# Optimization experiments

Measured on AMD Instinct MI355X. Metric: run time of the kernel, lower is better.

The kernel has to match this reference:

```python
import jax, jax.numpy as jnp
import numpy as np

N = 50000
E = 800000
F_IN = 128
HID = 64
HEADS = 4
NUM_TYPES = 1
NEG_SLOPE = 0.2


def setup_inputs() -> dict:
    key = jax.random.key(0)
    ks = jax.random.split(key, 20)
    s = 0.05
    inp = {
        "node_features": jax.random.normal(ks[0], (N, F_IN), jnp.float32),
        "node_types": jax.random.randint(ks[1], (N,), 0, NUM_TYPES, jnp.int32),
        "edge_index": jax.random.randint(ks[2], (2, E), 0, N, jnp.int32),
        # params
        "type_emb": jax.random.normal(ks[3], (NUM_TYPES, HID), jnp.float32) * s,
        "proj_w": jax.random.normal(ks[4], (F_IN, HID), jnp.float32) * s,
        "proj_b": jnp.zeros((HID,), jnp.float32),
        # GAT layer 0: in=64 -> heads*64, concat=True
        "lin_w0": jax.random.normal(ks[5], (HID, HEADS * HID), jnp.float32) * s,
        "att_src0": jax.random.normal(ks[6], (HEADS, HID), jnp.float32) * s,
        "att_dst0": jax.random.normal(ks[7], (HEADS, HID), jnp.float32) * s,
        "bias0": jnp.zeros((HEADS * HID,), jnp.float32),
        "ln_g0": jnp.ones((HEADS * HID,), jnp.float32),
        "ln_b0": jnp.zeros((HEADS * HID,), jnp.float32),
        # GAT layer 1: in=256 -> heads*64, concat=False (mean over heads)
        "lin_w1": jax.random.normal(ks[8], (HEADS * HID, HEADS * HID), jnp.float32) * s,
        "att_src1": jax.random.normal(ks[9], (HEADS, HID), jnp.float32) * s,
        "att_dst1": jax.random.normal(ks[10], (HEADS, HID), jnp.float32) * s,
        "bias1": jnp.zeros((HID,), jnp.float32),
        "ln_g1": jnp.ones((HID,), jnp.float32),
        "ln_b1": jnp.zeros((HID,), jnp.float32),
    }
    return inp


def _layer_norm(x, g, b, eps=1e-5):
    mu = jnp.mean(x, axis=-1, keepdims=True)
    var = jnp.mean(jnp.square(x - mu), axis=-1, keepdims=True)
    return (x - mu) * jax.lax.rsqrt(var + eps) * g + b


def _gat_conv(x, src, dst, lin_w, att_src, att_dst, bias, concat):
    # PyG GATConv: linear -> per-edge additive attention -> segment softmax over
    # incoming edges -> weighted scatter-sum. Self-loops already in src/dst.
    n = x.shape[0]
    H, C = att_src.shape
    h = (x @ lin_w).reshape(n, H, C)            # [N,H,C]
    a_s = jnp.sum(h * att_src[None], axis=-1)   # [N,H]
    a_d = jnp.sum(h * att_dst[None], axis=-1)   # [N,H]
    a = jax.nn.leaky_relu(a_s[src] + a_d[dst], NEG_SLOPE)  # [E,H]
    m = jax.ops.segment_max(a, dst, num_segments=n)
    e = jnp.exp(a - m[dst])
    z = jax.ops.segment_sum(e, dst, num_segments=n)
    alpha = e / z[dst]                           # [E,H]
    msg = h[src] * alpha[..., None]              # [E,H,C]
    out = jax.ops.segment_sum(msg, dst, num_segments=n)  # [N,H,C]
    if concat:
        out = out.reshape(n, H * C)
    else:
        out = out.mean(axis=1)
    return out + bias


def reference(node_features, node_types, edge_index,
              type_emb, proj_w, proj_b,
              lin_w0, att_src0, att_dst0, bias0, ln_g0, ln_b0,
              lin_w1, att_src1, att_dst1, bias1, ln_g1, ln_b1):
    n = node_features.shape[0]
    # add self loops (PyG GATConv default add_self_loops=True)
    loop = jnp.arange(n, dtype=edge_index.dtype)
    src = jnp.concatenate([edge_index[0], loop])
    dst = jnp.concatenate([edge_index[1], loop])

    x = node_features @ proj_w + proj_b + type_emb[node_types]  # [N,64]

    # layer 0: no residual (i == 0)
    x = _gat_conv(x, src, dst, lin_w0, att_src0, att_dst0, bias0, concat=True)
    x = jax.nn.relu(_layer_norm(x, ln_g0, ln_b0))  # [N,256]; dropout = identity (eval)

    # layer 1: residual shape [N,256] != output [N,64] -> residual skipped
    x = _gat_conv(x, src, dst, lin_w1, att_src1, att_dst1, bias1, concat=False)
    x = jax.nn.relu(_layer_norm(x, ln_g1, ln_b1))  # [N,64]
    return x
```

## Files before the change

kernel.cpp:

```cpp
#include <hip/hip_runtime.h>


#define BLK 256
#define FB  2048

typedef __bf16 bf16x8 __attribute__((ext_vector_type(8)));
typedef __bf16 bf16x4 __attribute__((ext_vector_type(4)));
typedef float  f32x4  __attribute__((ext_vector_type(4)));


__device__ __forceinline__ void pack_body(const float* __restrict__ w,
                                          __bf16* __restrict__ wp,
                                          int K, int NC, int idx) {
  const int tot = (K >> 3) * NC;
  if (idx >= tot) return;
  int g = idx / NC, c = idx - g * NC;
#pragma unroll
  for (int j = 0; j < 8; ++j)
    wp[(size_t)idx * 8 + j] = (__bf16)w[(g * 8 + j) * NC + c];
}

__device__ __forceinline__ void proj_body(
    int bid, const float* __restrict__ nf, const int* __restrict__ types,
    const __bf16* __restrict__ pwp, const float* __restrict__ pb,
    const float* __restrict__ emb, __bf16* __restrict__ x0, int n) {
  const int t = threadIdx.x, w = t >> 6, l = t & 63;
  const int l15 = l & 15, lg = l >> 4;
  const int mbase = bid * 64 + w * 16;
  f32x4 acc[4] = {};
  const int ar = mbase + l15;
  const bool av = ar < n;
#pragma unroll
  for (int ks = 0; ks < 4; ++ks) {
    bf16x8 a = {};
    if (av) {
      const float* ap = nf + (size_t)ar * 128 + ks * 32 + lg * 8;
      float4 f0 = *(const float4*)(ap);
      float4 f1 = *(const float4*)(ap + 4);
      a[0] = (__bf16)f0.x; a[1] = (__bf16)f0.y; a[2] = (__bf16)f0.z; a[3] = (__bf16)f0.w;
      a[4] = (__bf16)f1.x; a[5] = (__bf16)f1.y; a[6] = (__bf16)f1.z; a[7] = (__bf16)f1.w;
    }
#pragma unroll
    for (int nt = 0; nt < 4; ++nt) {
      int c = nt * 16 + l15;
      int g = ks * 4 + lg;
      bf16x8 b = *(const bf16x8*)(pwp + ((size_t)g * 64 + c) * 8);
      acc[nt] = __builtin_amdgcn_mfma_f32_16x16x32_bf16(a, b, acc[nt], 0, 0, 0);
    }
  }
#pragma unroll
  for (int reg = 0; reg < 4; ++reg) {
    int row = mbase + lg * 4 + reg;
    if (row < n) {
      int ty = types[row];
#pragma unroll
      for (int nt = 0; nt < 4; ++nt) {
        int c = nt * 16 + l15;
        x0[(size_t)row * 64 + c] = (__bf16)(acc[nt][reg] + pb[c] + emb[ty * 64 + c]);
      }
    }
  }
}

template <int K>
__device__ __forceinline__ void lin_body(
    int bid, const __bf16* __restrict__ X, const __bf16* __restrict__ Wp,
    const float* __restrict__ att_s, const float* __restrict__ att_d,
    __bf16* __restrict__ H, float* __restrict__ as_, float* __restrict__ ad_, int n) {
  const int t = threadIdx.x, w = t >> 6, l = t & 63;
  const int l15 = l & 15, lg = l >> 4;
  const int m0 = bid * 64;

  float asv[4], adv[4];
#pragma unroll
  for (int nt = 0; nt < 4; ++nt) {
    int c = w * 64 + nt * 16 + l15;
    asv[nt] = att_s[c];
    adv[nt] = att_d[c];
  }

  f32x4 acc[4][4] = {};
  int rr[4];
  bool vv[4];
#pragma unroll
  for (int mt = 0; mt < 4; ++mt) { rr[mt] = m0 + mt * 16 + l15; vv[mt] = rr[mt] < n; }
  const bf16x8 zf = {};

  for (int ks = 0; ks < K / 32; ++ks) {
    bf16x8 a[4];
#pragma unroll
    for (int mt = 0; mt < 4; ++mt)
      a[mt] = vv[mt] ? *(const bf16x8*)(X + (size_t)rr[mt] * K + ks * 32 + lg * 8) : zf;
    bf16x8 b[4];
#pragma unroll
    for (int nt = 0; nt < 4; ++nt) {
      int c = w * 64 + nt * 16 + l15;
      int g = ks * 4 + lg;
      b[nt] = *(const bf16x8*)(Wp + ((size_t)g * 256 + c) * 8);
    }
#pragma unroll
    for (int nt = 0; nt < 4; ++nt)
#pragma unroll
      for (int mt = 0; mt < 4; ++mt)
        acc[mt][nt] = __builtin_amdgcn_mfma_f32_16x16x32_bf16(a[mt], b[nt], acc[mt][nt], 0, 0, 0);
  }

#pragma unroll
  for (int mt = 0; mt < 4; ++mt) {
#pragma unroll
    for (int reg = 0; reg < 4; ++reg) {
      int row = m0 + mt * 16 + lg * 4 + reg;
      bool vr = row < n;
      float s = 0.f, d = 0.f;
      if (vr) {
#pragma unroll
        for (int nt = 0; nt < 4; ++nt) {
          float cv = acc[mt][nt][reg];
          H[(size_t)row * 256 + w * 64 + nt * 16 + l15] = (__bf16)cv;
          s = fmaf(cv, asv[nt], s);
          d = fmaf(cv, adv[nt], d);
        }
      }
#pragma unroll
      for (int o = 8; o; o >>= 1) { s += __shfl_xor(s, o); d += __shfl_xor(d, o); }
      if (l15 == 0 && vr) { as_[row * 4 + w] = s; ad_[row * 4 + w] = d; }
    }
  }
}


__global__ __launch_bounds__(BLK) void k_prep(
    const float* __restrict__ pw, const float* __restrict__ w0,
    const float* __restrict__ w1, __bf16* __restrict__ pwp,
    __bf16* __restrict__ w0p, __bf16* __restrict__ w1p,
    int* __restrict__ cnt, int* __restrict__ sidx, int n, int nchunks) {
  int b = blockIdx.x;
  const int t = threadIdx.x;
  if (b < nchunks) {
    int i = b * BLK + t;
    if (i < n) { cnt[i] = 1; sidx[(size_t)i << 6] = i; }
    return;
  }
  b -= nchunks;
  if (b < 4)  { pack_body(pw, pwp, 128, 64,  b * BLK + t); return; }
  b -= 4;
  if (b < 8)  { pack_body(w0, w0p, 64, 256,  b * BLK + t); return; }
  b -= 8;
  pack_body(w1, w1p, 256, 256, b * BLK + t);
}

__global__ __launch_bounds__(BLK) void k_fill_proj(
    const int* __restrict__ src, const int* __restrict__ dst,
    int* __restrict__ cnt, int* __restrict__ sidx, int E,
    const float* __restrict__ nf, const int* __restrict__ types,
    const __bf16* __restrict__ pwp, const float* __restrict__ pb,
    const float* __restrict__ emb, __bf16* __restrict__ x0, int n) {
  if (blockIdx.x < FB) {
    for (int e = blockIdx.x * BLK + threadIdx.x; e < E; e += FB * BLK) {
      int s = src[e], d = dst[e];
      int slot = atomicAdd(&cnt[d], 1);
      if (slot < 64) sidx[((size_t)d << 6) + slot] = s;
    }
    return;
  }
  proj_body(blockIdx.x - FB, nf, types, pwp, pb, emb, x0, n);
}

__global__ __launch_bounds__(BLK) void k_lin64(
    const __bf16* __restrict__ X, const __bf16* __restrict__ Wp,
    const float* __restrict__ att_s, const float* __restrict__ att_d,
    __bf16* __restrict__ H, float* __restrict__ as_, float* __restrict__ ad_, int n) {
  lin_body<64>(blockIdx.x, X, Wp, att_s, att_d, H, as_, ad_, n);
}

__global__ __launch_bounds__(BLK) void k_lin256(
    const __bf16* __restrict__ X, const __bf16* __restrict__ Wp,
    const float* __restrict__ att_s, const float* __restrict__ att_d,
    __bf16* __restrict__ H, float* __restrict__ as_, float* __restrict__ ad_, int n) {
  lin_body<256>(blockIdx.x, X, Wp, att_s, att_d, H, as_, ad_, n);
}


__global__ __launch_bounds__(BLK) void k_agg0(
    const int* __restrict__ cntA, const int* __restrict__ sidx,
    const float* __restrict__ as_, const float* __restrict__ ad_,
    const __bf16* __restrict__ h0,
    const float* __restrict__ bias, const float* __restrict__ g,
    const float* __restrict__ b, __bf16* __restrict__ x1, int n) {
  const int lane = threadIdx.x & 63;
  const int wid = (blockIdx.x * BLK + threadIdx.x) >> 6;
  const int nw = (gridDim.x * BLK) >> 6;
  const int hsel = lane >> 4;
  const float4 bias4 = ((const float4*)bias)[lane];
  const float4 g4 = ((const float4*)g)[lane];
  const float4 b4 = ((const float4*)b)[lane];
  for (int d = wid; d < n; d += nw) {
    int cnt = cntA[d]; if (cnt > 64) cnt = 64;
    const int* sp = sidx + ((size_t)d << 6);
    const float adv = ad_[d * 4 + hsel];
    float ax = 0.f, ay = 0.f, az = 0.f, aw = 0.f, z = 0.f;
    int j = 0;
    for (; j + 4 <= cnt; j += 4) {
      int4 s4 = *(const int4*)(sp + j);
      int s0 = __builtin_amdgcn_readfirstlane(s4.x);
      int s1 = __builtin_amdgcn_readfirstlane(s4.y);
      int s2 = __builtin_amdgcn_readfirstlane(s4.z);
      int s3 = __builtin_amdgcn_readfirstlane(s4.w);
      float q0 = as_[s0 * 4 + hsel], q1 = as_[s1 * 4 + hsel];
      float q2 = as_[s2 * 4 + hsel], q3 = as_[s3 * 4 + hsel];
      bf16x4 v0 = *(const bf16x4*)(h0 + (size_t)s0 * 256 + lane * 4);
      bf16x4 v1 = *(const bf16x4*)(h0 + (size_t)s1 * 256 + lane * 4);
      bf16x4 v2 = *(const bf16x4*)(h0 + (size_t)s2 * 256 + lane * 4);
      bf16x4 v3 = *(const bf16x4*)(h0 + (size_t)s3 * 256 + lane * 4);
      float a;
      a = q0 + adv; a = fmaxf(a, 0.2f * a); float e0 = __expf(a);
      a = q1 + adv; a = fmaxf(a, 0.2f * a); float e1 = __expf(a);
      a = q2 + adv; a = fmaxf(a, 0.2f * a); float e2 = __expf(a);
      a = q3 + adv; a = fmaxf(a, 0.2f * a); float e3 = __expf(a);
      z += (e0 + e1) + (e2 + e3);
      ax = fmaf(e0, (float)v0[0], ax); ay = fmaf(e0, (float)v0[1], ay);
      az = fmaf(e0, (float)v0[2], az); aw = fmaf(e0, (float)v0[3], aw);
      ax = fmaf(e1, (float)v1[0], ax); ay = fmaf(e1, (float)v1[1], ay);
      az = fmaf(e1, (float)v1[2], az); aw = fmaf(e1, (float)v1[3], aw);
      ax = fmaf(e2, (float)v2[0], ax); ay = fmaf(e2, (float)v2[1], ay);
      az = fmaf(e2, (float)v2[2], az); aw = fmaf(e2, (float)v2[3], aw);
      ax = fmaf(e3, (float)v3[0], ax); ay = fmaf(e3, (float)v3[1], ay);
      az = fmaf(e3, (float)v3[2], az); aw = fmaf(e3, (float)v3[3], aw);
    }
    for (; j < cnt; ++j) {
      int s = __builtin_amdgcn_readfirstlane(sp[j]);
      float a = as_[s * 4 + hsel] + adv; a = fmaxf(a, 0.2f * a);
      float e = __expf(a);
      z += e;
      bf16x4 hv = *(const bf16x4*)(h0 + (size_t)s * 256 + lane * 4);
      ax = fmaf(e, (float)hv[0], ax); ay = fmaf(e, (float)hv[1], ay);
      az = fmaf(e, (float)hv[2], az); aw = fmaf(e, (float)hv[3], aw);
    }
    float rz = 1.f / z;
    float vx = ax * rz + bias4.x, vy = ay * rz + bias4.y;
    float vz = az * rz + bias4.z, vw = aw * rz + bias4.w;
    float s1 = vx + vy + vz + vw;
#pragma unroll
    for (int o = 32; o; o >>= 1) s1 += __shfl_xor(s1, o);
    float mu = s1 * (1.f / 256.f);
    float dx = vx - mu, dy = vy - mu, dz = vz - mu, dw = vw - mu;
    float q = dx * dx + dy * dy + dz * dz + dw * dw;
#pragma unroll
    for (int o = 32; o; o >>= 1) q += __shfl_xor(q, o);
    float is = rsqrtf(q * (1.f / 256.f) + 1e-5f);
    bf16x4 o4;
    o4[0] = (__bf16)fmaxf(dx * is * g4.x + b4.x, 0.f);
    o4[1] = (__bf16)fmaxf(dy * is * g4.y + b4.y, 0.f);
    o4[2] = (__bf16)fmaxf(dz * is * g4.z + b4.z, 0.f);
    o4[3] = (__bf16)fmaxf(dw * is * g4.w + b4.w, 0.f);
    *(bf16x4*)(x1 + (size_t)d * 256 + lane * 4) = o4;
  }
}

__global__ __launch_bounds__(BLK) void k_agg1(
    const int* __restrict__ cntA, const int* __restrict__ sidx,
    const float* __restrict__ as_, const float* __restrict__ ad_,
    const __bf16* __restrict__ h1,
    const float* __restrict__ bias, const float* __restrict__ g,
    const float* __restrict__ b, float* __restrict__ out, int n) {
  const int lane = threadIdx.x & 63;
  const int wid = (blockIdx.x * BLK + threadIdx.x) >> 6;
  const int nw = (gridDim.x * BLK) >> 6;
  const int hsel = lane >> 4;
  const int p = lane & 15;
  const float4 bias4 = ((const float4*)bias)[p];
  const float4 g4 = ((const float4*)g)[p];
  const float4 b4 = ((const float4*)b)[p];
  for (int d = wid; d < n; d += nw) {
    int cnt = cntA[d]; if (cnt > 64) cnt = 64;
    const int* sp = sidx + ((size_t)d << 6);
    const float adv = ad_[d * 4 + hsel];
    float ax = 0.f, ay = 0.f, az = 0.f, aw = 0.f, z = 0.f;
    int j = 0;
    for (; j + 4 <= cnt; j += 4) {
      int4 s4 = *(const int4*)(sp + j);
      int s0 = __builtin_amdgcn_readfirstlane(s4.x);
      int s1 = __builtin_amdgcn_readfirstlane(s4.y);
      int s2 = __builtin_amdgcn_readfirstlane(s4.z);
      int s3 = __builtin_amdgcn_readfirstlane(s4.w);
      float q0 = as_[s0 * 4 + hsel], q1 = as_[s1 * 4 + hsel];
      float q2 = as_[s2 * 4 + hsel], q3 = as_[s3 * 4 + hsel];
      bf16x4 v0 = *(const bf16x4*)(h1 + (size_t)s0 * 256 + lane * 4);
      bf16x4 v1 = *(const bf16x4*)(h1 + (size_t)s1 * 256 + lane * 4);
      bf16x4 v2 = *(const bf16x4*)(h1 + (size_t)s2 * 256 + lane * 4);
      bf16x4 v3 = *(const bf16x4*)(h1 + (size_t)s3 * 256 + lane * 4);
      float a;
      a = q0 + adv; a = fmaxf(a, 0.2f * a); float e0 = __expf(a);
      a = q1 + adv; a = fmaxf(a, 0.2f * a); float e1 = __expf(a);
      a = q2 + adv; a = fmaxf(a, 0.2f * a); float e2 = __expf(a);
      a = q3 + adv; a = fmaxf(a, 0.2f * a); float e3 = __expf(a);
      z += (e0 + e1) + (e2 + e3);
      ax = fmaf(e0, (float)v0[0], ax); ay = fmaf(e0, (float)v0[1], ay);
      az = fmaf(e0, (float)v0[2], az); aw = fmaf(e0, (float)v0[3], aw);
      ax = fmaf(e1, (float)v1[0], ax); ay = fmaf(e1, (float)v1[1], ay);
      az = fmaf(e1, (float)v1[2], az); aw = fmaf(e1, (float)v1[3], aw);
      ax = fmaf(e2, (float)v2[0], ax); ay = fmaf(e2, (float)v2[1], ay);
      az = fmaf(e2, (float)v2[2], az); aw = fmaf(e2, (float)v2[3], aw);
      ax = fmaf(e3, (float)v3[0], ax); ay = fmaf(e3, (float)v3[1], ay);
      az = fmaf(e3, (float)v3[2], az); aw = fmaf(e3, (float)v3[3], aw);
    }
    for (; j < cnt; ++j) {
      int s = __builtin_amdgcn_readfirstlane(sp[j]);
      float a = as_[s * 4 + hsel] + adv; a = fmaxf(a, 0.2f * a);
      float e = __expf(a);
      z += e;
      bf16x4 hv = *(const bf16x4*)(h1 + (size_t)s * 256 + lane * 4);
      ax = fmaf(e, (float)hv[0], ax); ay = fmaf(e, (float)hv[1], ay);
      az = fmaf(e, (float)hv[2], az); aw = fmaf(e, (float)hv[3], aw);
    }
    float rz = 1.f / z;
    ax *= rz; ay *= rz; az *= rz; aw *= rz;
#pragma unroll
    for (int o = 16; o <= 32; o <<= 1) {
      ax += __shfl_xor(ax, o); ay += __shfl_xor(ay, o);
      az += __shfl_xor(az, o); aw += __shfl_xor(aw, o);
    }
    float vx = 0.25f * ax + bias4.x, vy = 0.25f * ay + bias4.y;
    float vz = 0.25f * az + bias4.z, vw = 0.25f * aw + bias4.w;
    float s1 = vx + vy + vz + vw;
#pragma unroll
    for (int o = 8; o; o >>= 1) s1 += __shfl_xor(s1, o);
    float mu = s1 * (1.f / 64.f);
    float dx = vx - mu, dy = vy - mu, dz = vz - mu, dw = vw - mu;
    float q = dx * dx + dy * dy + dz * dz + dw * dw;
#pragma unroll
    for (int o = 8; o; o >>= 1) q += __shfl_xor(q, o);
    float is = rsqrtf(q * (1.f / 64.f) + 1e-5f);
    if (lane < 16) {
      float4 o4;
      o4.x = fmaxf(dx * is * g4.x + b4.x, 0.f);
      o4.y = fmaxf(dy * is * g4.y + b4.y, 0.f);
      o4.z = fmaxf(dz * is * g4.z + b4.z, 0.f);
      o4.w = fmaxf(dw * is * g4.w + b4.w, 0.f);
      ((float4*)(out + (size_t)d * 64))[p] = o4;
    }
  }
}

extern "C" void kernel_launch(void* const* d_in, const int* in_sizes, int n_in,
                              void* d_out, int out_size, void* d_ws, size_t ws_size,
                              hipStream_t stream) {
  const float* nf    = (const float*)d_in[0];
  const int*   types = (const int*)d_in[1];
  const int*   ei    = (const int*)d_in[2];
  const float* emb   = (const float*)d_in[3];
  const float* pw    = (const float*)d_in[4];
  const float* pb    = (const float*)d_in[5];
  const float* w0    = (const float*)d_in[6];
  const float* asrc0 = (const float*)d_in[7];
  const float* adst0 = (const float*)d_in[8];
  const float* b0    = (const float*)d_in[9];
  const float* g0    = (const float*)d_in[10];
  const float* be0   = (const float*)d_in[11];
  const float* w1    = (const float*)d_in[12];
  const float* asrc1 = (const float*)d_in[13];
  const float* adst1 = (const float*)d_in[14];
  const float* b1    = (const float*)d_in[15];
  const float* g1    = (const float*)d_in[16];
  const float* be1   = (const float*)d_in[17];

  const int n = in_sizes[0] / 128;
  const int E = in_sizes[2] / 2;
  const int* srcI = ei;
  const int* dstI = ei + E;

  float* W = (float*)d_ws;
  size_t o = 0;
  __bf16* x0  = (__bf16*)(W + o); o += (size_t)n * 32;
  __bf16* h   = (__bf16*)(W + o); o += (size_t)n * 128;
  __bf16* x1  = (__bf16*)(W + o); o += (size_t)n * 128;
  float* as_ = W + o;             o += (size_t)n * 4;
  float* ad_ = W + o;             o += (size_t)n * 4;
  __bf16* w0p = (__bf16*)(W + o); o += 64 * 256 / 2;
  __bf16* w1p = (__bf16*)(W + o); o += 256 * 256 / 2;
  __bf16* pwp = (__bf16*)(W + o); o += 128 * 64 / 2;
  int* I = (int*)(W + o);
  size_t io = 0;
  int* cnt  = I + io; io += n;
  int* sidx = I + io; io += (size_t)n * 64;

  const int nchunks = (n + BLK - 1) / BLK;
  const int mgrid = (n + 63) / 64;
  const int agrid = (n * 64 + BLK - 1) / BLK;

  k_prep<<<nchunks + 44, BLK, 0, stream>>>(pw, w0, w1, pwp, w0p, w1p, cnt, sidx, n, nchunks);
  k_fill_proj<<<FB + mgrid, BLK, 0, stream>>>(srcI, dstI, cnt, sidx, E,
                                              nf, types, pwp, pb, emb, x0, n);
  k_lin64<<<mgrid, BLK, 0, stream>>>(x0, w0p, asrc0, adst0, h, as_, ad_, n);
  k_agg0<<<agrid, BLK, 0, stream>>>(cnt, sidx, as_, ad_, h, b0, g0, be0, x1, n);
  k_lin256<<<mgrid, BLK, 0, stream>>>(x1, w1p, asrc1, adst1, h, as_, ad_, n);
  k_agg1<<<agrid, BLK, 0, stream>>>(cnt, sidx, as_, ad_, h, b1, g1, be1,
                                    (float*)d_out, n);
}
```

Before: 258.1 us.

## Fuse input projection with layer-0 linear via LDS and batch edge-fill atomics

Merges the input projection and the layer-0 GAT linear into one kernel. The projected 64-wide tile is staged in shared memory instead of being written to and reread from global memory, which removes one launch and the x0 round trip. The edge-fill part now uses fewer blocks and issues four independent edge loads and atomics per thread iteration to raise memory-level parallelism. The trade-off is extra LDS use and possibly lower occupancy for the projection blocks, and fewer fill blocks may reduce overlap with the MFMA work.

```diff
diff --git a/kernel.cpp b/kernel.cpp
--- a/kernel.cpp
+++ b/kernel.cpp
@@ -2,7 +2,7 @@
 
 
 #define BLK 256
-#define FB  2048
+#define FB  768
 
 typedef __bf16 bf16x8 __attribute__((ext_vector_type(8)));
 typedef __bf16 bf16x4 __attribute__((ext_vector_type(4)));
@@ -18,114 +18,6 @@
 #pragma unroll
   for (int j = 0; j < 8; ++j)
     wp[(size_t)idx * 8 + j] = (__bf16)w[(g * 8 + j) * NC + c];
-}
-
-__device__ __forceinline__ void proj_body(
-    int bid, const float* __restrict__ nf, const int* __restrict__ types,
-    const __bf16* __restrict__ pwp, const float* __restrict__ pb,
-    const float* __restrict__ emb, __bf16* __restrict__ x0, int n) {
-  const int t = threadIdx.x, w = t >> 6, l = t & 63;
-  const int l15 = l & 15, lg = l >> 4;
-  const int mbase = bid * 64 + w * 16;
-  f32x4 acc[4] = {};
-  const int ar = mbase + l15;
-  const bool av = ar < n;
-#pragma unroll
-  for (int ks = 0; ks < 4; ++ks) {
-    bf16x8 a = {};
-    if (av) {
-      const float* ap = nf + (size_t)ar * 128 + ks * 32 + lg * 8;
-      float4 f0 = *(const float4*)(ap);
-      float4 f1 = *(const float4*)(ap + 4);
-      a[0] = (__bf16)f0.x; a[1] = (__bf16)f0.y; a[2] = (__bf16)f0.z; a[3] = (__bf16)f0.w;
-      a[4] = (__bf16)f1.x; a[5] = (__bf16)f1.y; a[6] = (__bf16)f1.z; a[7] = (__bf16)f1.w;
-    }
-#pragma unroll
-    for (int nt = 0; nt < 4; ++nt) {
-      int c = nt * 16 + l15;
-      int g = ks * 4 + lg;
-      bf16x8 b = *(const bf16x8*)(pwp + ((size_t)g * 64 + c) * 8);
-      acc[nt] = __builtin_amdgcn_mfma_f32_16x16x32_bf16(a, b, acc[nt], 0, 0, 0);
-    }
-  }
-#pragma unroll
-  for (int reg = 0; reg < 4; ++reg) {
-    int row = mbase + lg * 4 + reg;
-    if (row < n) {
-      int ty = types[row];
-#pragma unroll
-      for (int nt = 0; nt < 4; ++nt) {
-        int c = nt * 16 + l15;
-        x0[(size_t)row * 64 + c] = (__bf16)(acc[nt][reg] + pb[c] + emb[ty * 64 + c]);
-      }
-    }
-  }
-}
-
-template <int K>
-__device__ __forceinline__ void lin_body(
-    int bid, const __bf16* __restrict__ X, const __bf16* __restrict__ Wp,
-    const float* __restrict__ att_s, const float* __restrict__ att_d,
-    __bf16* __restrict__ H, float* __restrict__ as_, float* __restrict__ ad_, int n) {
-  const int t = threadIdx.x, w = t >> 6, l = t & 63;
-  const int l15 = l & 15, lg = l >> 4;
-  const int m0 = bid * 64;
-
-  float asv[4], adv[4];
-#pragma unroll
-  for (int nt = 0; nt < 4; ++nt) {
-    int c = w * 64 + nt * 16 + l15;
-    asv[nt] = att_s[c];
-    adv[nt] = att_d[c];
-  }
-
-  f32x4 acc[4][4] = {};
-  int rr[4];
-  bool vv[4];
-#pragma unroll
-  for (int mt = 0; mt < 4; ++mt) { rr[mt] = m0 + mt * 16 + l15; vv[mt] = rr[mt] < n; }
-  const bf16x8 zf = {};
-
-  for (int ks = 0; ks < K / 32; ++ks) {
-    bf16x8 a[4];
-#pragma unroll
-    for (int mt = 0; mt < 4; ++mt)
-      a[mt] = vv[mt] ? *(const bf16x8*)(X + (size_t)rr[mt] * K + ks * 32 + lg * 8) : zf;
-    bf16x8 b[4];
-#pragma unroll
-    for (int nt = 0; nt < 4; ++nt) {
-      int c = w * 64 + nt * 16 + l15;
-      int g = ks * 4 + lg;
-      b[nt] = *(const bf16x8*)(Wp + ((size_t)g * 256 + c) * 8);
-    }
-#pragma unroll
-    for (int nt = 0; nt < 4; ++nt)
-#pragma unroll
-      for (int mt = 0; mt < 4; ++mt)
-        acc[mt][nt] = __builtin_amdgcn_mfma_f32_16x16x32_bf16(a[mt], b[nt], acc[mt][nt], 0, 0, 0);
-  }
-
-#pragma unroll
-  for (int mt = 0; mt < 4; ++mt) {
-#pragma unroll
-    for (int reg = 0; reg < 4; ++reg) {
-      int row = m0 + mt * 16 + lg * 4 + reg;
-      bool vr = row < n;
-      float s = 0.f, d = 0.f;
-      if (vr) {
-#pragma unroll
-        for (int nt = 0; nt < 4; ++nt) {
-          float cv = acc[mt][nt][reg];
-          H[(size_t)row * 256 + w * 64 + nt * 16 + l15] = (__bf16)cv;
-          s = fmaf(cv, asv[nt], s);
-          d = fmaf(cv, adv[nt], d);
-        }
-      }
-#pragma unroll
-      for (int o = 8; o; o >>= 1) { s += __shfl_xor(s, o); d += __shfl_xor(d, o); }
-      if (l15 == 0 && vr) { as_[row * 4 + w] = s; ad_[row * 4 + w] = d; }
-    }
-  }
 }
 
 
@@ -149,35 +41,197 @@
   pack_body(w1, w1p, 256, 256, b * BLK + t);
 }
 
-__global__ __launch_bounds__(BLK) void k_fill_proj(
+__global__ __launch_bounds__(BLK) void k_fill_projlin0(
     const int* __restrict__ src, const int* __restrict__ dst,
     int* __restrict__ cnt, int* __restrict__ sidx, int E,
     const float* __restrict__ nf, const int* __restrict__ types,
     const __bf16* __restrict__ pwp, const float* __restrict__ pb,
-    const float* __restrict__ emb, __bf16* __restrict__ x0, int n) {
+    const float* __restrict__ emb,
+    const __bf16* __restrict__ w0p,
+    const float* __restrict__ asrc0, const float* __restrict__ adst0,
+    __bf16* __restrict__ H, float* __restrict__ as_, float* __restrict__ ad_,
+    int n) {
+  __shared__ __bf16 xt[64][72];
   if (blockIdx.x < FB) {
-    for (int e = blockIdx.x * BLK + threadIdx.x; e < E; e += FB * BLK) {
-      int s = src[e], d = dst[e];
-      int slot = atomicAdd(&cnt[d], 1);
-      if (slot < 64) sidx[((size_t)d << 6) + slot] = s;
+    const int st = FB * BLK;
+    for (int e = blockIdx.x * BLK + threadIdx.x; e < E; e += 4 * st) {
+      const int e1 = e + st, e2 = e + 2 * st, e3 = e + 3 * st;
+      const bool vB = e1 < E, vC = e2 < E, vD = e3 < E;
+      int sA = src[e], dA = dst[e];
+      int sB = 0, dB = 0, sC = 0, dC = 0, sD = 0, dD = 0;
+      if (vB) { sB = src[e1]; dB = dst[e1]; }
+      if (vC) { sC = src[e2]; dC = dst[e2]; }
+      if (vD) { sD = src[e3]; dD = dst[e3]; }
+      int slA = atomicAdd(&cnt[dA], 1);
+      int slB = vB ? atomicAdd(&cnt[dB], 1) : 64;
+      int slC = vC ? atomicAdd(&cnt[dC], 1) : 64;
+      int slD = vD ? atomicAdd(&cnt[dD], 1) : 64;
+      if (slA < 64) sidx[((size_t)dA << 6) + slA] = sA;
+      if (slB < 64) sidx[((size_t)dB << 6) + slB] = sB;
+      if (slC < 64) sidx[((size_t)dC << 6) + slC] = sC;
+      if (slD < 64) sidx[((size_t)dD << 6) + slD] = sD;
     }
     return;
   }
-  proj_body(blockIdx.x - FB, nf, types, pwp, pb, emb, x0, n);
-}
-
-__global__ __launch_bounds__(BLK) void k_lin64(
-    const __bf16* __restrict__ X, const __bf16* __restrict__ Wp,
-    const float* __restrict__ att_s, const float* __restrict__ att_d,
-    __bf16* __restrict__ H, float* __restrict__ as_, float* __restrict__ ad_, int n) {
-  lin_body<64>(blockIdx.x, X, Wp, att_s, att_d, H, as_, ad_, n);
+  const int bid = blockIdx.x - FB;
+  const int t = threadIdx.x, w = t >> 6, l = t & 63;
+  const int l15 = l & 15, lg = l >> 4;
+  const int m0 = bid * 64;
+
+  {
+    const int mbase = m0 + w * 16;
+    f32x4 acc[4] = {};
+    const int ar = mbase + l15;
+    const bool av = ar < n;
+#pragma unroll
+    for (int ks = 0; ks < 4; ++ks) {
+      bf16x8 a = {};
+      if (av) {
+        const float* ap = nf + (size_t)ar * 128 + ks * 32 + lg * 8;
+        float4 f0 = *(const float4*)(ap);
+        float4 f1 = *(const float4*)(ap + 4);
+        a[0] = (__bf16)f0.x; a[1] = (__bf16)f0.y; a[2] = (__bf16)f0.z; a[3] = (__bf16)f0.w;
+        a[4] = (__bf16)f1.x; a[5] = (__bf16)f1.y; a[6] = (__bf16)f1.z; a[7] = (__bf16)f1.w;
+      }
+#pragma unroll
+      for (int nt = 0; nt < 4; ++nt) {
+        int c = nt * 16 + l15;
+        int g = ks * 4 + lg;
+        bf16x8 b = *(const bf16x8*)(pwp + ((size_t)g * 64 + c) * 8);
+        acc[nt] = __builtin_amdgcn_mfma_f32_16x16x32_bf16(a, b, acc[nt], 0, 0, 0);
+      }
+    }
+#pragma unroll
+    for (int reg = 0; reg < 4; ++reg) {
+      int row = mbase + lg * 4 + reg;
+      int lrow = w * 16 + lg * 4 + reg;
+      if (row < n) {
+        int ty = types[row];
+#pragma unroll
+        for (int nt = 0; nt < 4; ++nt) {
+          int c = nt * 16 + l15;
+          xt[lrow][c] = (__bf16)(acc[nt][reg] + pb[c] + emb[ty * 64 + c]);
+        }
+      } else {
+#pragma unroll
+        for (int nt = 0; nt < 4; ++nt) xt[lrow][nt * 16 + l15] = (__bf16)0.f;
+      }
+    }
+  }
+  __syncthreads();
+
+  float asv[4], adv[4];
+#pragma unroll
+  for (int nt = 0; nt < 4; ++nt) {
+    int c = w * 64 + nt * 16 + l15;
+    asv[nt] = asrc0[c];
+    adv[nt] = adst0[c];
+  }
+  f32x4 acc[4][4] = {};
+  for (int ks = 0; ks < 2; ++ks) {
+    bf16x8 a[4];
+#pragma unroll
+    for (int mt = 0; mt < 4; ++mt)
+      a[mt] = *(const bf16x8*)&xt[mt * 16 + l15][ks * 32 + lg * 8];
+    bf16x8 b[4];
+#pragma unroll
+    for (int nt = 0; nt < 4; ++nt) {
+      int c = w * 64 + nt * 16 + l15;
+      int g = ks * 4 + lg;
+      b[nt] = *(const bf16x8*)(w0p + ((size_t)g * 256 + c) * 8);
+    }
+#pragma unroll
+    for (int nt = 0; nt < 4; ++nt)
+#pragma unroll
+      for (int mt = 0; mt < 4; ++mt)
+        acc[mt][nt] = __builtin_amdgcn_mfma_f32_16x16x32_bf16(a[mt], b[nt], acc[mt][nt], 0, 0, 0);
+  }
+#pragma unroll
+  for (int mt = 0; mt < 4; ++mt) {
+#pragma unroll
+    for (int reg = 0; reg < 4; ++reg) {
+      int row = m0 + mt * 16 + lg * 4 + reg;
+      bool vr = row < n;
+      float s = 0.f, d = 0.f;
+      if (vr) {
+#pragma unroll
+        for (int nt = 0; nt < 4; ++nt) {
+          float cv = acc[mt][nt][reg];
+          H[(size_t)row * 256 + w * 64 + nt * 16 + l15] = (__bf16)cv;
+          s = fmaf(cv, asv[nt], s);
+          d = fmaf(cv, adv[nt], d);
+        }
+      }
+#pragma unroll
+      for (int o = 8; o; o >>= 1) { s += __shfl_xor(s, o); d += __shfl_xor(d, o); }
+      if (l15 == 0 && vr) { as_[row * 4 + w] = s; ad_[row * 4 + w] = d; }
+    }
+  }
 }
 
 __global__ __launch_bounds__(BLK) void k_lin256(
     const __bf16* __restrict__ X, const __bf16* __restrict__ Wp,
     const float* __restrict__ att_s, const float* __restrict__ att_d,
     __bf16* __restrict__ H, float* __restrict__ as_, float* __restrict__ ad_, int n) {
-  lin_body<256>(blockIdx.x, X, Wp, att_s, att_d, H, as_, ad_, n);
+  const int t = threadIdx.x, w = t >> 6, l = t & 63;
+  const int l15 = l & 15, lg = l >> 4;
+  const int m0 = blockIdx.x * 64;
+
+  float asv[4], adv[4];
+#pragma unroll
+  for (int nt = 0; nt < 4; ++nt) {
+    int c = w * 64 + nt * 16 + l15;
+    asv[nt] = att_s[c];
+    adv[nt] = att_d[c];
+  }
+
+  f32x4 acc[4][4] = {};
+  int rr[4];
+  bool vv[4];
+#pragma unroll
+  for (int mt = 0; mt < 4; ++mt) { rr[mt] = m0 + mt * 16 + l15; vv[mt] = rr[mt] < n; }
+  const bf16x8 zf = {};
+
+  for (int ks = 0; ks < 8; ++ks) {
+    bf16x8 a[4];
+#pragma unroll
+    for (int mt = 0; mt < 4; ++mt)
+      a[mt] = vv[mt] ? *(const bf16x8*)(X + (size_t)rr[mt] * 256 + ks * 32 + lg * 8) : zf;
+    bf16x8 b[4];
+#pragma unroll
+    for (int nt = 0; nt < 4; ++nt) {
+      int c = w * 64 + nt * 16 + l15;
+      int g = ks * 4 + lg;
+      b[nt] = *(const bf16x8*)(Wp + ((size_t)g * 256 + c) * 8);
+    }
+#pragma unroll
+    for (int nt = 0; nt < 4; ++nt)
+#pragma unroll
+      for (int mt = 0; mt < 4; ++mt)
+        acc[mt][nt] = __builtin_amdgcn_mfma_f32_16x16x32_bf16(a[mt], b[nt], acc[mt][nt], 0, 0, 0);
+  }
+
+#pragma unroll
+  for (int mt = 0; mt < 4; ++mt) {
+#pragma unroll
+    for (int reg = 0; reg < 4; ++reg) {
+      int row = m0 + mt * 16 + lg * 4 + reg;
+      bool vr = row < n;
+      float s = 0.f, d = 0.f;
+      if (vr) {
+#pragma unroll
+        for (int nt = 0; nt < 4; ++nt) {
+          float cv = acc[mt][nt][reg];
+          H[(size_t)row * 256 + w * 64 + nt * 16 + l15] = (__bf16)cv;
+          s = fmaf(cv, asv[nt], s);
+          d = fmaf(cv, adv[nt], d);
+        }
+      }
+#pragma unroll
+      for (int o = 8; o; o >>= 1) { s += __shfl_xor(s, o); d += __shfl_xor(d, o); }
+      if (l15 == 0 && vr) { as_[row * 4 + w] = s; ad_[row * 4 + w] = d; }
+    }
+  }
 }
 
 
@@ -371,7 +425,6 @@
 
   float* W = (float*)d_ws;
   size_t o = 0;
-  __bf16* x0  = (__bf16*)(W + o); o += (size_t)n * 32;
   __bf16* h   = (__bf16*)(W + o); o += (size_t)n * 128;
   __bf16* x1  = (__bf16*)(W + o); o += (size_t)n * 128;
   float* as_ = W + o;             o += (size_t)n * 4;
@@ -389,9 +442,9 @@
   const int agrid = (n * 64 + BLK - 1) / BLK;
 
   k_prep<<<nchunks + 44, BLK, 0, stream>>>(pw, w0, w1, pwp, w0p, w1p, cnt, sidx, n, nchunks);
-  k_fill_proj<<<FB + mgrid, BLK, 0, stream>>>(srcI, dstI, cnt, sidx, E,
-                                              nf, types, pwp, pb, emb, x0, n);
-  k_lin64<<<mgrid, BLK, 0, stream>>>(x0, w0p, asrc0, adst0, h, as_, ad_, n);
+  k_fill_projlin0<<<FB + mgrid, BLK, 0, stream>>>(srcI, dstI, cnt, sidx, E,
+                                                  nf, types, pwp, pb, emb,
+                                                  w0p, asrc0, adst0, h, as_, ad_, n);
   k_agg0<<<agrid, BLK, 0, stream>>>(cnt, sidx, as_, ad_, h, b0, g0, be0, x1, n);
   k_lin256<<<mgrid, BLK, 0, stream>>>(x1, w1p, asrc1, adst1, h, as_, ad_, n);
   k_agg1<<<agrid, BLK, 0, stream>>>(cnt, sidx, as_, ad_, h, b1, g1, be1,
```

Result: faster. 247.8 us (-4.0%).
